# Optimization experiments

Measured on AMD Instinct MI355X. Metric: run time of the kernel, lower is better.

Reference implementation:

```python
import jax, jax.numpy as jnp
import numpy as np

K = 2  # top-k

def setup_inputs() -> dict:
    key = jax.random.key(0)
    k1, k2, k3, k4, k5 = jax.random.split(key, 5)
    B, D, E = 32768, 4096, 64
    return {
        "x": jax.random.normal(k1, (B, D), dtype=jnp.float32),
        "gate_w": jax.random.normal(k2, (D, E), dtype=jnp.float32) * 0.02,
        "gate_b": jax.random.normal(k3, (E,), dtype=jnp.float32) * 0.02,
        "w_noise": jax.random.normal(k4, (D, E), dtype=jnp.float32) * 0.02,
        "noise": jax.random.normal(k5, (B, E), dtype=jnp.float32),
    }

def reference(x, gate_w, gate_b, w_noise, noise):
    B = x.shape[0]
    E = gate_w.shape[1]
    clean_logits = x @ gate_w + gate_b                      # [B, E]
    noise_logits = x @ w_noise                              # [B, E]
    logits = clean_logits + noise * jax.nn.softplus(noise_logits)
    probs = jax.nn.softmax(logits, axis=1)                  # [B, E]
    top_k_vals, top_k_indices = jax.lax.top_k(logits, K)    # [B, K]
    top_k_gates = jax.nn.softmax(top_k_vals, axis=1)        # [B, K]
    importance = probs.sum(axis=0)                          # [E]
    rows = jnp.arange(B)[:, None]                           # [B, 1]
    mask = jnp.zeros((B, E), dtype=x.dtype).at[rows, top_k_indices].set(1.0)
    load = mask.sum(axis=0)                                 # [E]
    aux_loss = (importance * load).mean() * (E ** 2)
    return top_k_gates, top_k_indices, aux_loss
```

## Files before the change

kernel.cpp:

```cpp
#include <hip/hip_runtime.h>
#include <hip/hip_bf16.h>
#include <math.h>

#define BROWS 32768
#define DDIM  4096
#define NEXP  64
#define NCOL  128
#define BM    128
#define BK    64
#define LDA   72
#define NK    (DDIM / BK)

typedef __attribute__((ext_vector_type(8))) short  short8;
typedef __attribute__((ext_vector_type(4))) float  float4v;

static __device__ __forceinline__ unsigned int f2bf_u(float f) {
    union { float f; unsigned int u; } v; v.f = f;
    unsigned int r = v.u + 0x7FFFu + ((v.u >> 16) & 1u);
    return r >> 16;
}
static __device__ __forceinline__ unsigned int pk2(float a, float b) {
    return f2bf_u(a) | (f2bf_u(b) << 16);
}

__global__ void bt_prepass(const float* __restrict__ gw, const float* __restrict__ wn,
                           unsigned short* __restrict__ Bt) {
    int tid = blockIdx.x * 256 + threadIdx.x;
    int k = tid & (DDIM - 1);
    int n = tid >> 12;
    float v = (n < NEXP) ? gw[(size_t)k * NEXP + n] : wn[(size_t)k * NEXP + (n - NEXP)];
    Bt[(size_t)n * DDIM + k] = (unsigned short)f2bf_u(v);
}

__global__ __launch_bounds__(256, 1) void moe_main(
    const float* __restrict__ x, const float* __restrict__ gate_b,
    const float* __restrict__ noise, const unsigned short* __restrict__ Bt,
    float* __restrict__ out_gates, float* __restrict__ out_idx,
    float* __restrict__ g_imp, float* __restrict__ g_load)
{
    __shared__ char smem_raw[73728 + 512];
    unsigned short* As = (unsigned short*)smem_raw;
    unsigned short* Bs = As + 2 * 128 * LDA;
    float* Lq   = (float*)smem_raw;
    float* impP = (float*)(smem_raw + 73728);
    float* ldP  = impP + 64;

    const int tid  = threadIdx.x;
    const int row0 = blockIdx.x * BM;

    const int sm = tid >> 1;
    const int sh = tid & 1;
    const float*          xa = x  + (size_t)(row0 + sm) * DDIM + sh * 32;
    const unsigned short* bg = Bt + (size_t)sm * DDIM + sh * 32;

    const int wv   = tid >> 6;
    const int ln   = tid & 63;
    const int q    = ln >> 4;
    const int l15  = ln & 15;
    const int wrow = (wv >> 1) * 64;
    const int wcol = (wv & 1) * 64;

    float4 av[8];
    uint4  bv[4];
    float4v acc[4][4];
#pragma unroll
    for (int i = 0; i < 4; ++i)
#pragma unroll
        for (int j = 0; j < 4; ++j) acc[i][j] = (float4v)0.f;

    {
        const float4* ap = (const float4*)(xa);
        const uint4*  bp = (const uint4*)(bg);
#pragma unroll
        for (int i = 0; i < 8; ++i) av[i] = ap[i];
#pragma unroll
        for (int i = 0; i < 4; ++i) bv[i] = bp[i];
        unsigned short* ad = As + sm * LDA + sh * 32;
        unsigned short* bd = Bs + sm * LDA + sh * 32;
#pragma unroll
        for (int i = 0; i < 4; ++i) {
            uint4 w;
            w.x = pk2(av[2*i].x, av[2*i].y);
            w.y = pk2(av[2*i].z, av[2*i].w);
            w.z = pk2(av[2*i+1].x, av[2*i+1].y);
            w.w = pk2(av[2*i+1].z, av[2*i+1].w);
            ((uint4*)ad)[i] = w;
            ((uint4*)bd)[i] = bv[i];
        }
    }
    __syncthreads();

    for (int c = 0; c < NK; ++c) {
        const int cur = (c & 1) * 128 * LDA;
        if (c + 1 < NK) {
            const float4* ap = (const float4*)(xa + (size_t)(c + 1) * BK);
            const uint4*  bp = (const uint4*)(bg + (size_t)(c + 1) * BK);
#pragma unroll
            for (int i = 0; i < 8; ++i) av[i] = ap[i];
#pragma unroll
            for (int i = 0; i < 4; ++i) bv[i] = bp[i];
        }
        {
            const unsigned short* ab = As + cur + (wrow + l15) * LDA + q * 8;
            const unsigned short* bb = Bs + cur + (wcol + l15) * LDA + q * 8;
#pragma unroll
            for (int s = 0; s < 2; ++s) {
                short8 af[4], bfr[4];
#pragma unroll
                for (int mt = 0; mt < 4; ++mt)
                    af[mt] = *(const short8*)(ab + mt * 16 * LDA + s * 32);
#pragma unroll
                for (int nt = 0; nt < 4; ++nt)
                    bfr[nt] = *(const short8*)(bb + nt * 16 * LDA + s * 32);
#pragma unroll
                for (int mt = 0; mt < 4; ++mt)
#pragma unroll
                    for (int nt = 0; nt < 4; ++nt)
                        acc[mt][nt] = __builtin_amdgcn_mfma_f32_16x16x32_bf16(
                            af[mt], bfr[nt], acc[mt][nt], 0, 0, 0);
            }
        }
        if (c + 1 < NK) {
            const int nxt = ((c + 1) & 1) * 128 * LDA;
            unsigned short* ad = As + nxt + sm * LDA + sh * 32;
            unsigned short* bd = Bs + nxt + sm * LDA + sh * 32;
#pragma unroll
            for (int i = 0; i < 4; ++i) {
                uint4 w;
                w.x = pk2(av[2*i].x, av[2*i].y);
                w.y = pk2(av[2*i].z, av[2*i].w);
                w.z = pk2(av[2*i+1].x, av[2*i+1].y);
                w.w = pk2(av[2*i+1].z, av[2*i+1].w);
                ((uint4*)ad)[i] = w;
                ((uint4*)bd)[i] = bv[i];
            }
        }
        __syncthreads();
    }

    float* Ldst = Lq + (wv & 1) * (128 * 66);
#pragma unroll
    for (int mt = 0; mt < 4; ++mt)
#pragma unroll
        for (int nt = 0; nt < 4; ++nt)
#pragma unroll
            for (int r = 0; r < 4; ++r) {
                int m = wrow + mt * 16 + q * 4 + r;
                int n = nt * 16 + l15;
                Ldst[m * 66 + n] = acc[mt][nt][r];
            }
    if (tid < 128) ((float*)(smem_raw + 73728))[tid] = 0.f;
    __syncthreads();

    const float* Lc = Lq;
    const float* Ln = Lq + 128 * 66;
    const int e = ln;
    const float gb = gate_b[e];
    float imp_acc = 0.f, load_acc = 0.f;

    for (int r32 = 0; r32 < 32; ++r32) {
        const int m = wv * 32 + r32;
        float cl = Lc[m * 66 + e] + gb;
        float nz = Ln[m * 66 + e];
        float nv = noise[(size_t)(row0 + m) * NEXP + e];
        float sp = (nz > 0.f) ? (nz + log1pf(expf(-nz))) : log1pf(expf(nz));
        float lg = cl + nv * sp;

        float v1 = lg, v2 = -INFINITY;
        int   i1 = e,  i2 = 127;
#pragma unroll
        for (int msk = 1; msk < 64; msk <<= 1) {
            float o1 = __shfl_xor(v1, msk, 64);
            int  oi1 = __shfl_xor(i1, msk, 64);
            float o2 = __shfl_xor(v2, msk, 64);
            int  oi2 = __shfl_xor(i2, msk, 64);
            bool ofirst = (o1 > v1) || (o1 == v1 && oi1 < i1);
            if (ofirst) {
                bool t2 = (v1 > o2) || (v1 == o2 && i1 < oi2);
                v2 = t2 ? v1 : o2;  i2 = t2 ? i1 : oi2;
                v1 = o1;            i1 = oi1;
            } else {
                bool t2 = (o1 > v2) || (o1 == v2 && oi1 < i2);
                v2 = t2 ? o1 : v2;  i2 = t2 ? oi1 : i2;
            }
        }
        float p = expf(lg - v1);
        float s = p;
#pragma unroll
        for (int msk = 1; msk < 64; msk <<= 1) s += __shfl_xor(s, msk, 64);
        imp_acc += p / s;
        load_acc += (e == i1 ? 1.f : 0.f) + (e == i2 ? 1.f : 0.f);

        if (ln == 0) {
            float g1 = 1.f / (1.f + expf(v2 - v1));
            size_t r = (size_t)(row0 + m) * 2;
            out_gates[r]     = g1;
            out_gates[r + 1] = 1.f - g1;
            out_idx[r]     = (float)i1;
            out_idx[r + 1] = (float)i2;
        }
    }
    atomicAdd(&impP[e], imp_acc);
    atomicAdd(&ldP[e], load_acc);
    __syncthreads();
    if (tid < 64) {
        atomicAdd(&g_imp[tid], impP[tid]);
        atomicAdd(&g_load[tid], ldP[tid]);
    }
}

__global__ void aux_k(const float* __restrict__ imp, const float* __restrict__ ld,
                      float* __restrict__ out) {
    int e = threadIdx.x;
    float s = imp[e] * ld[e];
#pragma unroll
    for (int msk = 1; msk < 64; msk <<= 1) s += __shfl_xor(s, msk, 64);
    if (e == 0) out[0] = s * 64.f;
}

extern "C" void kernel_launch(void* const* d_in, const int* in_sizes, int n_in,
                              void* d_out, int out_size, void* d_ws, size_t ws_size,
                              hipStream_t stream) {
    const float* x     = (const float*)d_in[0];
    const float* gw    = (const float*)d_in[1];
    const float* gb    = (const float*)d_in[2];
    const float* wn    = (const float*)d_in[3];
    const float* noise = (const float*)d_in[4];
    float* out = (float*)d_out;

    float* g_imp  = (float*)d_ws;
    float* g_load = g_imp + 64;
    unsigned short* Bt = (unsigned short*)((char*)d_ws + 1024);

    hipMemsetAsync(d_ws, 0, 512, stream);
    bt_prepass<<<dim3((NCOL * DDIM) / 256), dim3(256), 0, stream>>>(gw, wn, Bt);
    moe_main<<<dim3(BROWS / BM), dim3(256), 0, stream>>>(
        x, gb, noise, Bt, out, out + (size_t)BROWS * 2, g_imp, g_load);
    aux_k<<<dim3(1), dim3(64), 0, stream>>>(g_imp, g_load, out + (size_t)BROWS * 4);
}
```

Before: 813.7 us.

## Restructure router GEMM into single-wave 16-row blocks without LDS staging

The router kernel is rewritten so that each 64-thread block handles 16 rows and all 128 output columns. Each lane loads its MFMA fragments directly from global memory into registers with one-step register prefetch, which removes the LDS double-buffer and the per-K-step barriers. The fp32-to-bf16 conversion becomes a truncating byte-permute instead of round-to-nearest. Block-level LDS atomics are replaced by direct global atomics. Each block now re-reads the full 1 MB bf16 weight matrix, so B traffic to L2 rises sharply. There are 2048 blocks issuing global atomics, and truncation changes numerics slightly, which could flip top-k ties.

Result: slower. 942.7 us (+15.8%).

```diff
diff --git a/kernel.cpp b/kernel.cpp
--- a/kernel.cpp
+++ b/kernel.cpp
@@ -1,15 +1,11 @@
 #include <hip/hip_runtime.h>
-#include <hip/hip_bf16.h>
 #include <math.h>
 
 #define BROWS 32768
 #define DDIM  4096
 #define NEXP  64
-#define NCOL  128
-#define BM    128
-#define BK    64
-#define LDA   72
-#define NK    (DDIM / BK)
+#define NSTEP 128
+#define LSTR  132
 
 typedef __attribute__((ext_vector_type(8))) short  short8;
 typedef __attribute__((ext_vector_type(4))) float  float4v;
@@ -19,8 +15,10 @@
     unsigned int r = v.u + 0x7FFFu + ((v.u >> 16) & 1u);
     return r >> 16;
 }
-static __device__ __forceinline__ unsigned int pk2(float a, float b) {
-    return f2bf_u(a) | (f2bf_u(b) << 16);
+
+static __device__ __forceinline__ unsigned int pk_perm(float lo, float hi) {
+    union { float f; unsigned int u; } a, b; a.f = lo; b.f = hi;
+    return __builtin_amdgcn_perm(b.u, a.u, 0x07060302u);
 }
 
 __global__ void bt_prepass(const float* __restrict__ gw, const float* __restrict__ wn,
@@ -32,136 +30,80 @@
     Bt[(size_t)n * DDIM + k] = (unsigned short)f2bf_u(v);
 }
 
-__global__ __launch_bounds__(256, 1) void moe_main(
+__global__ __launch_bounds__(64) void moe_router(
     const float* __restrict__ x, const float* __restrict__ gate_b,
     const float* __restrict__ noise, const unsigned short* __restrict__ Bt,
     float* __restrict__ out_gates, float* __restrict__ out_idx,
     float* __restrict__ g_imp, float* __restrict__ g_load)
 {
-    __shared__ char smem_raw[73728 + 512];
-    unsigned short* As = (unsigned short*)smem_raw;
-    unsigned short* Bs = As + 2 * 128 * LDA;
-    float* Lq   = (float*)smem_raw;
-    float* impP = (float*)(smem_raw + 73728);
-    float* ldP  = impP + 64;
+    __shared__ float Lw[16][LSTR];
 
-    const int tid  = threadIdx.x;
-    const int row0 = blockIdx.x * BM;
+    const int ln  = threadIdx.x;
+    const int q   = ln >> 4;
+    const int l15 = ln & 15;
+    const int row0 = blockIdx.x * 16;
 
-    const int sm = tid >> 1;
-    const int sh = tid & 1;
-    const float*          xa = x  + (size_t)(row0 + sm) * DDIM + sh * 32;
-    const unsigned short* bg = Bt + (size_t)sm * DDIM + sh * 32;
+    const float4* ap = (const float4*)(x + (size_t)(row0 + l15) * DDIM + q * 8);
+    const uint4*  bp = (const uint4*)(Bt + (size_t)l15 * DDIM + q * 8);
 
-    const int wv   = tid >> 6;
-    const int ln   = tid & 63;
-    const int q    = ln >> 4;
-    const int l15  = ln & 15;
-    const int wrow = (wv >> 1) * 64;
-    const int wcol = (wv & 1) * 64;
+    float4v acc[8];
+#pragma unroll
+    for (int nt = 0; nt < 8; ++nt) acc[nt] = (float4v)0.f;
 
-    float4 av[8];
-    uint4  bv[4];
-    float4v acc[4][4];
+    float4 a0, a1, na0, na1;
+    uint4  b[8], nb[8];
+
+    a0 = ap[0]; a1 = ap[1];
 #pragma unroll
-    for (int i = 0; i < 4; ++i)
+    for (int nt = 0; nt < 8; ++nt) b[nt] = bp[(size_t)nt * 8192];
+
+    for (int s = 0; s < NSTEP - 1; ++s) {
+        na0 = ap[(s + 1) * 8];
+        na1 = ap[(s + 1) * 8 + 1];
 #pragma unroll
-        for (int j = 0; j < 4; ++j) acc[i][j] = (float4v)0.f;
+        for (int nt = 0; nt < 8; ++nt) nb[nt] = bp[(size_t)nt * 8192 + (s + 1) * 4];
 
+        union { uint4 u; short8 s8; } pa;
+        pa.u.x = pk_perm(a0.x, a0.y);
+        pa.u.y = pk_perm(a0.z, a0.w);
+        pa.u.z = pk_perm(a1.x, a1.y);
+        pa.u.w = pk_perm(a1.z, a1.w);
+#pragma unroll
+        for (int nt = 0; nt < 8; ++nt) {
+            union { uint4 u; short8 s8; } pb; pb.u = b[nt];
+            acc[nt] = __builtin_amdgcn_mfma_f32_16x16x32_bf16(pa.s8, pb.s8, acc[nt], 0, 0, 0);
+        }
+        a0 = na0; a1 = na1;
+#pragma unroll
+        for (int nt = 0; nt < 8; ++nt) b[nt] = nb[nt];
+    }
     {
-        const float4* ap = (const float4*)(xa);
-        const uint4*  bp = (const uint4*)(bg);
+        union { uint4 u; short8 s8; } pa;
+        pa.u.x = pk_perm(a0.x, a0.y);
+        pa.u.y = pk_perm(a0.z, a0.w);
+        pa.u.z = pk_perm(a1.x, a1.y);
+        pa.u.w = pk_perm(a1.z, a1.w);
 #pragma unroll
-        for (int i = 0; i < 8; ++i) av[i] = ap[i];
-#pragma unroll
-        for (int i = 0; i < 4; ++i) bv[i] = bp[i];
-        unsigned short* ad = As + sm * LDA + sh * 32;
-        unsigned short* bd = Bs + sm * LDA + sh * 32;
-#pragma unroll
-        for (int i = 0; i < 4; ++i) {
-            uint4 w;
-            w.x = pk2(av[2*i].x, av[2*i].y);
-            w.y = pk2(av[2*i].z, av[2*i].w);
-            w.z = pk2(av[2*i+1].x, av[2*i+1].y);
-            w.w = pk2(av[2*i+1].z, av[2*i+1].w);
-            ((uint4*)ad)[i] = w;
-            ((uint4*)bd)[i] = bv[i];
+        for (int nt = 0; nt < 8; ++nt) {
+            union { uint4 u; short8 s8; } pb; pb.u = b[nt];
+            acc[nt] = __builtin_amdgcn_mfma_f32_16x16x32_bf16(pa.s8, pb.s8, acc[nt], 0, 0, 0);
         }
     }
+
+#pragma unroll
+    for (int nt = 0; nt < 8; ++nt)
+#pragma unroll
+        for (int r = 0; r < 4; ++r)
+            Lw[q * 4 + r][nt * 16 + l15] = acc[nt][r];
     __syncthreads();
 
-    for (int c = 0; c < NK; ++c) {
-        const int cur = (c & 1) * 128 * LDA;
-        if (c + 1 < NK) {
-            const float4* ap = (const float4*)(xa + (size_t)(c + 1) * BK);
-            const uint4*  bp = (const uint4*)(bg + (size_t)(c + 1) * BK);
-#pragma unroll
-            for (int i = 0; i < 8; ++i) av[i] = ap[i];
-#pragma unroll
-            for (int i = 0; i < 4; ++i) bv[i] = bp[i];
-        }
-        {
-            const unsigned short* ab = As + cur + (wrow + l15) * LDA + q * 8;
-            const unsigned short* bb = Bs + cur + (wcol + l15) * LDA + q * 8;
-#pragma unroll
-            for (int s = 0; s < 2; ++s) {
-                short8 af[4], bfr[4];
-#pragma unroll
-                for (int mt = 0; mt < 4; ++mt)
-                    af[mt] = *(const short8*)(ab + mt * 16 * LDA + s * 32);
-#pragma unroll
-                for (int nt = 0; nt < 4; ++nt)
-                    bfr[nt] = *(const short8*)(bb + nt * 16 * LDA + s * 32);
-#pragma unroll
-                for (int mt = 0; mt < 4; ++mt)
-#pragma unroll
-                    for (int nt = 0; nt < 4; ++nt)
-                        acc[mt][nt] = __builtin_amdgcn_mfma_f32_16x16x32_bf16(
-                            af[mt], bfr[nt], acc[mt][nt], 0, 0, 0);
-            }
-        }
-        if (c + 1 < NK) {
-            const int nxt = ((c + 1) & 1) * 128 * LDA;
-            unsigned short* ad = As + nxt + sm * LDA + sh * 32;
-            unsigned short* bd = Bs + nxt + sm * LDA + sh * 32;
-#pragma unroll
-            for (int i = 0; i < 4; ++i) {
-                uint4 w;
-                w.x = pk2(av[2*i].x, av[2*i].y);
-                w.y = pk2(av[2*i].z, av[2*i].w);
-                w.z = pk2(av[2*i+1].x, av[2*i+1].y);
-                w.w = pk2(av[2*i+1].z, av[2*i+1].w);
-                ((uint4*)ad)[i] = w;
-                ((uint4*)bd)[i] = bv[i];
-            }
-        }
-        __syncthreads();
-    }
-
-    float* Ldst = Lq + (wv & 1) * (128 * 66);
-#pragma unroll
-    for (int mt = 0; mt < 4; ++mt)
-#pragma unroll
-        for (int nt = 0; nt < 4; ++nt)
-#pragma unroll
-            for (int r = 0; r < 4; ++r) {
-                int m = wrow + mt * 16 + q * 4 + r;
-                int n = nt * 16 + l15;
-                Ldst[m * 66 + n] = acc[mt][nt][r];
-            }
-    if (tid < 128) ((float*)(smem_raw + 73728))[tid] = 0.f;
-    __syncthreads();
-
-    const float* Lc = Lq;
-    const float* Ln = Lq + 128 * 66;
     const int e = ln;
-    const float gb = gate_b[e];
+    const float gbv = gate_b[e];
     float imp_acc = 0.f, load_acc = 0.f;
 
-    for (int r32 = 0; r32 < 32; ++r32) {
-        const int m = wv * 32 + r32;
-        float cl = Lc[m * 66 + e] + gb;
-        float nz = Ln[m * 66 + e];
+    for (int m = 0; m < 16; ++m) {
+        float cl = Lw[m][e] + gbv;
+        float nz = Lw[m][64 + e];
         float nv = noise[(size_t)(row0 + m) * NEXP + e];
         float sp = (nz > 0.f) ? (nz + log1pf(expf(-nz))) : log1pf(expf(nz));
         float lg = cl + nv * sp;
@@ -185,28 +127,23 @@
             }
         }
         float p = expf(lg - v1);
-        float s = p;
+        float ssum = p;
 #pragma unroll
-        for (int msk = 1; msk < 64; msk <<= 1) s += __shfl_xor(s, msk, 64);
-        imp_acc += p / s;
+        for (int msk = 1; msk < 64; msk <<= 1) ssum += __shfl_xor(ssum, msk, 64);
+        imp_acc += p / ssum;
         load_acc += (e == i1 ? 1.f : 0.f) + (e == i2 ? 1.f : 0.f);
 
         if (ln == 0) {
             float g1 = 1.f / (1.f + expf(v2 - v1));
-            size_t r = (size_t)(row0 + m) * 2;
-            out_gates[r]     = g1;
-            out_gates[r + 1] = 1.f - g1;
-            out_idx[r]     = (float)i1;
-            out_idx[r + 1] = (float)i2;
+            size_t rr = (size_t)(row0 + m) * 2;
+            out_gates[rr]     = g1;
+            out_gates[rr + 1] = 1.f - g1;
+            out_idx[rr]     = (float)i1;
+            out_idx[rr + 1] = (float)i2;
         }
     }
-    atomicAdd(&impP[e], imp_acc);
-    atomicAdd(&ldP[e], load_acc);
-    __syncthreads();
-    if (tid < 64) {
-        atomicAdd(&g_imp[tid], impP[tid]);
-        atomicAdd(&g_load[tid], ldP[tid]);
-    }
+    atomicAdd(&g_imp[e], imp_acc);
+    atomicAdd(&g_load[e], load_acc);
 }
 
 __global__ void aux_k(const float* __restrict__ imp, const float* __restrict__ ld,
@@ -233,8 +170,8 @@
     unsigned short* Bt = (unsigned short*)((char*)d_ws + 1024);
 
     hipMemsetAsync(d_ws, 0, 512, stream);
-    bt_prepass<<<dim3((NCOL * DDIM) / 256), dim3(256), 0, stream>>>(gw, wn, Bt);
-    moe_main<<<dim3(BROWS / BM), dim3(256), 0, stream>>>(
+    bt_prepass<<<dim3((128 * DDIM) / 256), dim3(256), 0, stream>>>(gw, wn, Bt);
+    moe_router<<<dim3(BROWS / 16), dim3(64), 0, stream>>>(
         x, gb, noise, Bt, out, out + (size_t)BROWS * 2, g_imp, g_load);
     aux_k<<<dim3(1), dim3(64), 0, stream>>>(g_imp, g_load, out + (size_t)BROWS * 4);
 }
```
